# Kernel optimization log

Hardware: AMD Instinct MI355X
Metric: run time of the kernel (lower is better)

## Reference

```python
import jax, jax.numpy as jnp
import numpy as np

NEG_SLOPE = 0.2
EPS = 1e-5

N_NODES = 50000
N_GRAPHS = 500
NODES_PER_GRAPH = 100
N_EDGES = 500000
F_IN = 16
F_GRAPH = 4
HID = 64
N_CLASSES = 2


def setup_inputs() -> dict:
    key = jax.random.key(0)
    ks = jax.random.split(key, 32)
    x = jax.random.normal(ks[0], (N_NODES, F_IN), dtype=jnp.float32)
    # intra-graph random edges: dst lives in the same 100-node block as src
    src = jax.random.randint(ks[1], (N_EDGES,), 0, N_NODES)
    dst = (src // NODES_PER_GRAPH) * NODES_PER_GRAPH + jax.random.randint(ks[2], (N_EDGES,), 0, NODES_PER_GRAPH)
    edge_index = jnp.stack([src, dst]).astype(jnp.int64)
    graph_input = jax.random.normal(ks[3], (N_GRAPHS, F_GRAPH), dtype=jnp.float32)
    batch = (jnp.arange(N_NODES) // NODES_PER_GRAPH).astype(jnp.int64)

    def w(k, shape, scale=0.1):
        return (jax.random.normal(k, shape, dtype=jnp.float32) * scale)

    inp = dict(x=x, edge_index=edge_index, graph_input=graph_input, batch=batch)
    # GraphNorm params
    inp['gn_w'] = jnp.ones((F_IN,), jnp.float32)
    inp['gn_b'] = w(ks[4], (F_IN,))
    inp['gn_ms'] = jnp.ones((F_IN,), jnp.float32)
    inp['W1'] = w(ks[5], (F_IN, 4 * HID))
    inp['as1'] = w(ks[6], (4, HID)); inp['ad1'] = w(ks[7], (4, HID))
    inp['b1'] = w(ks[8], (4 * HID,))
    inp['W2'] = w(ks[9], (4 * HID, 4 * HID))
    inp['as2'] = w(ks[10], (4, HID)); inp['ad2'] = w(ks[11], (4, HID))
    inp['b2'] = w(ks[12], (4 * HID,))
    inp['W3'] = w(ks[13], (4 * HID, HID))
    inp['as3'] = w(ks[14], (1, HID)); inp['ad3'] = w(ks[15], (1, HID))
    inp['b3'] = w(ks[16], (HID,))
    # BatchNorm1d (eval mode) over [HID + F_GRAPH]
    D = HID + F_GRAPH
    inp['bn_g'] = 1.0 + w(ks[17], (D,))
    inp['bn_b'] = w(ks[18], (D,))
    inp['bn_m'] = jnp.zeros((D,), jnp.float32)
    inp['bn_v'] = jnp.ones((D,), jnp.float32)
    # Dense head
    inp['Wd1'] = w(ks[19], (D, HID)); inp['bd1'] = w(ks[20], (HID,))
    inp['Wd2'] = w(ks[21], (HID, HID)); inp['bd2'] = w(ks[22], (HID,))
    inp['Wo'] = w(ks[23], (HID, N_CLASSES)); inp['bo'] = w(ks[24], (N_CLASSES,))
    return inp


def _segment_softmax(e, seg, n):
    m = jax.ops.segment_max(e, seg, num_segments=n)
    ex = jnp.exp(e - m[seg])
    s = jax.ops.segment_sum(ex, seg, num_segments=n)
    return ex / s[seg]


def _gat_conv(x, src, dst, W, att_src, att_dst, b):
    N = x.shape[0]
    H, C = att_src.shape
    loop = jnp.arange(N)
    src = jnp.concatenate([src, loop])  # PyG GATConv adds self-loops
    dst = jnp.concatenate([dst, loop])
    h = (x @ W).reshape(N, H, C)
    a_src = (h * att_src).sum(-1)  # [N,H]
    a_dst = (h * att_dst).sum(-1)
    e = jax.nn.leaky_relu(a_src[src] + a_dst[dst], NEG_SLOPE)  # [E,H]
    alpha = _segment_softmax(e, dst, N)
    out = jax.ops.segment_sum(h[src] * alpha[:, :, None], dst, num_segments=N)
    return out.reshape(N, H * C) + b


def _graph_norm(x, batch, n_graphs, w, b, ms):
    cnt = jax.ops.segment_sum(jnp.ones((x.shape[0],), x.dtype), batch, num_segments=n_graphs)[:, None]
    mean = jax.ops.segment_sum(x, batch, num_segments=n_graphs) / cnt
    out = x - mean[batch] * ms
    var = jax.ops.segment_sum(out * out, batch, num_segments=n_graphs) / cnt
    return w * out / jnp.sqrt(var[batch] + EPS) + b


def _global_mean_pool(x, batch, n_graphs):
    cnt = jax.ops.segment_sum(jnp.ones((x.shape[0],), x.dtype), batch, num_segments=n_graphs)[:, None]
    return jax.ops.segment_sum(x, batch, num_segments=n_graphs) / cnt


def reference(x, edge_index, graph_input, batch,
              gn_w, gn_b, gn_ms,
              W1, as1, ad1, b1,
              W2, as2, ad2, b2,
              W3, as3, ad3, b3,
              bn_g, bn_b, bn_m, bn_v,
              Wd1, bd1, Wd2, bd2, Wo, bo):
    src, dst = edge_index[0], edge_index[1]
    G = graph_input.shape[0]
    h = _graph_norm(x, batch, G, gn_w, gn_b, gn_ms)
    # dropout is a no-op in eval
    h = jax.nn.elu(_gat_conv(h, src, dst, W1, as1, ad1, b1))
    h = jax.nn.elu(_gat_conv(h, src, dst, W2, as2, ad2, b2))
    h = _gat_conv(h, src, dst, W3, as3, ad3, b3)
    g = _global_mean_pool(h, batch, G)
    g = jnp.concatenate([g, graph_input], axis=1)
    g = (g - bn_m) / jnp.sqrt(bn_v + EPS) * bn_g + bn_b  # BatchNorm1d eval
    g = jax.nn.selu(g @ Wd1 + bd1)
    g = jax.nn.selu(g @ Wd2 + bd2)
    g = g @ Wo + bo
    return jax.nn.softmax(g, axis=1)
```

## Files before the change

### kernel.cpp

```cpp
#include <hip/hip_runtime.h>
#include <math.h>

#define N_NODES 50000
#define N_ROWS_PAD 50048
#define N_GRAPHS 500
#define NPG 100
#define N_EDGES 500000
#define F_IN 16
#define HID 64
#define EW_CAP 1408

#define SELU_SCALE 1.0507009873554804934193349852946f
#define SELU_ALPHA 1.6732632423543772848170429916717f

typedef __attribute__((ext_vector_type(8))) short short8;
typedef __attribute__((ext_vector_type(8))) unsigned short ushort8;
typedef __attribute__((ext_vector_type(4))) float floatx4;

__device__ __forceinline__ float lrelu(float x){ return x > 0.f ? x : 0.2f * x; }
__device__ __forceinline__ float eluf(float x){ return x > 0.f ? x : expf(x) - 1.f; }
__device__ __forceinline__ float seluf(float x){
    return x > 0.f ? SELU_SCALE * x : SELU_SCALE * (SELU_ALPHA * (expf(x) - 1.f));
}
__device__ __forceinline__ unsigned short f2bf(float x){
    unsigned u = __float_as_uint(x);
    return (unsigned short)((u + 0x7FFFu + ((u >> 16) & 1u)) >> 16);
}
__device__ __forceinline__ float bf2f(unsigned short u){
    return __uint_as_float((unsigned)u << 16);
}
__device__ __forceinline__ float bf2f_lo(unsigned u){
    return __uint_as_float(u << 16);
}
__device__ __forceinline__ float bf2f_hi(unsigned u){
    return __uint_as_float(u & 0xFFFF0000u);
}

__global__ void k_count(const int* __restrict__ dst, int* __restrict__ counts){
    int e = blockIdx.x * 256 + threadIdx.x;
    if (e < N_EDGES) atomicAdd(&counts[dst[e]], 1);
}

__global__ void __launch_bounds__(128)
k_local_scan(const int* __restrict__ counts, int* __restrict__ noff,
             int* __restrict__ cnt, int* __restrict__ write_ptr){
    __shared__ int s[128];
    int g = blockIdx.x, t = threadIdx.x;
    int v = (t < NPG) ? counts[g * NPG + t] : 0;
    s[t] = v; __syncthreads();
    for (int o = 1; o < 128; o <<= 1){
        int x = (t >= o) ? s[t - o] : 0;
        __syncthreads();
        s[t] += x;
        __syncthreads();
    }
    if (t < NPG){
        int excl = s[t] - v;
        noff[g * NPG + t] = excl;
        cnt[g * NPG + t] = v;
        write_ptr[g * NPG + t] = excl;
    }
}

__global__ void k_scatter(const int* __restrict__ src, const int* __restrict__ dst,
                          int* __restrict__ write_ptr, unsigned* __restrict__ csr){
    int e = blockIdx.x * 256 + threadIdx.x;
    if (e < N_EDGES){
        int d = dst[e];
        int g = d / NPG;
        int b = g * NPG;
        int pos = atomicAdd(&write_ptr[d], 1);
        csr[(size_t)g * EW_CAP + pos] = (unsigned)((src[e] - b) | ((d - b) << 8));
    }
}

__global__ void k_prep(const float* __restrict__ W1, const float* __restrict__ as1,
                       const float* __restrict__ ad1,
                       const float* __restrict__ W2, const float* __restrict__ as2,
                       const float* __restrict__ ad2,
                       const float* __restrict__ W3, const float* __restrict__ as3,
                       const float* __restrict__ ad3,
                       unsigned short* __restrict__ Wp2, unsigned short* __restrict__ Wp3,
                       float* __restrict__ M1f,
                       unsigned short* __restrict__ Mp2, unsigned short* __restrict__ Mp3){
    int id = blockIdx.x * 256 + threadIdx.x;
    if (id < 65536){
        int k = id >> 8, o = id & 255;
        int srccol = (o & 3) * 64 + (o >> 2);
        Wp2[(((k >> 3) * 256) + o) * 8 + (k & 7)] = f2bf(W2[k * 256 + srccol]);
    } else if (id < 81920){
        int i = id - 65536;
        int k = i >> 6, n = i & 63;
        Wp3[(((k >> 3) * 64) + n) * 8 + (k & 7)] = f2bf(W3[i]);
    } else if (id < 82048){
        int i = id - 81920;
        int k = i >> 3, j = i & 7;
        int h = j & 3;
        const float* a = (j < 4) ? as1 : ad1;
        float s = 0.f;
        for (int c = 0; c < 64; c++) s += W1[k * 256 + h * 64 + c] * a[h * 64 + c];
        M1f[k * 8 + j] = s;
    } else if (id < 86144){
        int i = id - 82048;
        int k = i >> 4, col = i & 15;
        float s = 0.f;
        if (col < 8){
            int h = col & 3;
            const float* a = (col < 4) ? as2 : ad2;
            for (int c = 0; c < 64; c++) s += W2[k * 256 + h * 64 + c] * a[h * 64 + c];
        }
        Mp2[((k >> 3) * 16 + col) * 8 + (k & 7)] = f2bf(s);
    } else if (id < 90240){
        int i = id - 86144;
        int k = i >> 4, col = i & 15;
        float s = 0.f;
        if (col < 2){
            const float* a = (col == 0) ? as3 : ad3;
            for (int c = 0; c < 64; c++) s += W3[k * 64 + c] * a[c];
        }
        Mp3[((k >> 3) * 16 + col) * 8 + (k & 7)] = f2bf(s);
    }
}

__global__ void __launch_bounds__(256)
k_gnorm_conv1(const float* __restrict__ x, const float* __restrict__ w,
              const float* __restrict__ b, const float* __restrict__ ms,
              const float* __restrict__ W1, const float* __restrict__ M1f,
              unsigned short* __restrict__ Ybf, float* __restrict__ lg1){
    __shared__ float sx[NPG * F_IN];
    __shared__ float Ws[16][256];
    __shared__ float red[16][16];
    __shared__ float meanS[16], varS[16];
    int g = blockIdx.x, t = threadIdx.x;
    int base = g * NPG;
    for (int idx = t; idx < NPG * F_IN; idx += 256) sx[idx] = x[base * F_IN + idx];
    for (int i = t; i < 1024; i += 256)
        *(float4*)&Ws[0][i * 4] = *(const float4*)&W1[i * 4];
    __syncthreads();
    int f = t & 15, grp = t >> 4;
    float p = 0.f;
    for (int i = grp; i < NPG; i += 16) p += sx[i * 16 + f];
    red[grp][f] = p; __syncthreads();
    if (t < 16){
        float s = 0.f;
        for (int i = 0; i < 16; i++) s += red[i][t];
        meanS[t] = s * (1.f / 100.f);
    }
    __syncthreads();
    float mm = meanS[f] * ms[f];
    p = 0.f;
    for (int i = grp; i < NPG; i += 16){ float v = sx[i * 16 + f] - mm; p += v * v; }
    red[grp][f] = p; __syncthreads();
    if (t < 16){
        float s = 0.f;
        for (int i = 0; i < 16; i++) s += red[i][t];
        varS[t] = s * (1.f / 100.f);
    }
    __syncthreads();
    for (int idx = t; idx < NPG * F_IN; idx += 256){
        int ff = idx & 15;
        sx[idx] = w[ff] * (sx[idx] - meanS[ff] * ms[ff]) * rsqrtf(varS[ff] + 1e-5f) + b[ff];
    }
    __syncthreads();
    int c4 = t & 15, rsub = t >> 4;
    for (int n = rsub; n < NPG; n += 16){
        float acc[16];
        #pragma unroll
        for (int j = 0; j < 16; j++) acc[j] = 0.f;
        #pragma unroll
        for (int k = 0; k < 16; k++){
            float a_ = sx[n * 16 + k];
            float4 b0 = *(const float4*)&Ws[k][c4 * 4];
            float4 b1 = *(const float4*)&Ws[k][64 + c4 * 4];
            float4 b2 = *(const float4*)&Ws[k][128 + c4 * 4];
            float4 b3 = *(const float4*)&Ws[k][192 + c4 * 4];
            float bv[16] = {b0.x, b0.y, b0.z, b0.w, b1.x, b1.y, b1.z, b1.w,
                            b2.x, b2.y, b2.z, b2.w, b3.x, b3.y, b3.z, b3.w};
            #pragma unroll
            for (int j = 0; j < 16; j++) acc[j] = fmaf(a_, bv[j], acc[j]);
        }
        ushort8 ua, ub;
        #pragma unroll
        for (int m = 0; m < 8; m++){
            ua[m] = f2bf(acc[(m & 3) * 4 + (m >> 2)]);
            ub[m] = f2bf(acc[(m & 3) * 4 + 2 + (m >> 2)]);
        }
        size_t ob = (size_t)(base + n) * 256 + c4 * 16;
        *(ushort8*)&Ybf[ob]     = ua;
        *(ushort8*)&Ybf[ob + 8] = ub;
    }
    for (int i = t; i < NPG * 8; i += 256){
        int n = i >> 3, j = i & 7;
        float s = 0.f;
        #pragma unroll
        for (int ff = 0; ff < 16; ff++) s += sx[n * 16 + ff] * M1f[ff * 8 + j];
        lg1[(size_t)(base + n) * 8 + j] = s;
    }
}

__global__ void __launch_bounds__(512)
k_fused4(const unsigned short* __restrict__ hbf, const float* __restrict__ lg,
         const float* __restrict__ bias,
         const unsigned* __restrict__ csr, const int* __restrict__ noff,
         const int* __restrict__ cnt, unsigned short* __restrict__ out_bf){
    __shared__ __align__(16) unsigned int edl[EW_CAP][4];
    __shared__ __align__(16) float asrcl[NPG * 4], adstl[NPG * 4];
    __shared__ __align__(16) float wselfl[NPG * 4], rsuml[NPG * 4];
    __shared__ int offl[NPG], cntl[NPG];

    int g = blockIdx.x, t = threadIdx.x;
    int wave = t >> 6, lane = t & 63;
    int base = g * NPG;
    size_t ebeg = (size_t)g * EW_CAP;

    if (t < NPG){
        offl[t] = noff[base + t];
        cntl[t] = cnt[base + t];
        const float* lp = lg + (size_t)(base + t) * 8;
        *(float4*)&asrcl[t * 4] = *(const float4*)lp;
        *(float4*)&adstl[t * 4] = *(const float4*)(lp + 4);
    }
    __syncthreads();
    int eln = offl[NPG - 1] + cntl[NPG - 1];
    for (int i = t; i < eln; i += 512) edl[i][2] = csr[ebeg + i];
    __syncthreads();

    for (int i = t; i < eln; i += 512){
        unsigned sd = edl[i][2];
        int s = sd & 0xFF, d = sd >> 8;
        float4 av = *(const float4*)&asrcl[s * 4];
        float4 dv = *(const float4*)&adstl[d * 4];
        unsigned w0 = f2bf(expf(lrelu(av.x + dv.x)));
        unsigned w1 = f2bf(expf(lrelu(av.y + dv.y)));
        unsigned w2 = f2bf(expf(lrelu(av.z + dv.z)));
        unsigned w3 = f2bf(expf(lrelu(av.w + dv.w)));
        edl[i][0] = w0 | (w1 << 16);
        edl[i][1] = w2 | (w3 << 16);
    }
    __syncthreads();

    if (t < NPG){
        int d = t;
        float4 av = *(const float4*)&asrcl[d * 4];
        float4 dv = *(const float4*)&adstl[d * 4];
        float ws0 = expf(lrelu(av.x + dv.x));
        float ws1 = expf(lrelu(av.y + dv.y));
        float ws2 = expf(lrelu(av.z + dv.z));
        float ws3 = expf(lrelu(av.w + dv.w));
        float s0 = ws0, s1 = ws1, s2 = ws2, s3 = ws3;
        int ebg = offl[d], n = cntl[d];
        for (int j = 0; j < n; j++){
            uint2 v = *(const uint2*)&edl[ebg + j][0];
            s0 += bf2f_lo(v.x); s1 += bf2f_hi(v.x);
            s2 += bf2f_lo(v.y); s3 += bf2f_hi(v.y);
        }
        *(float4*)&wselfl[d * 4] = make_float4(ws0, ws1, ws2, ws3);
        *(float4*)&rsuml[d * 4]  = make_float4(1.f / s0, 1.f / s1, 1.f / s2, 1.f / s3);
    }
    __syncthreads();

    float b0 = bias[lane], b1 = bias[64 + lane], b2 = bias[128 + lane], b3 = bias[192 + lane];
    for (int d = wave; d < NPG; d += 8){
        float4 ws = *(const float4*)&wselfl[d * 4];
        float4 rs = *(const float4*)&rsuml[d * 4];
        ushort4 hv = *(const ushort4*)&hbf[(size_t)(base + d) * 256 + lane * 4];
        float a0 = ws.x * bf2f(hv.x);
        float a1 = ws.y * bf2f(hv.y);
        float a2 = ws.z * bf2f(hv.z);
        float a3 = ws.w * bf2f(hv.w);
        int ebg = offl[d], n = cntl[d];
        int j = 0;
        #pragma unroll 1
        for (; j + 4 <= n; j += 4){
            #pragma unroll
            for (int k = 0; k < 4; k++){
                uint4 v = *(const uint4*)&edl[ebg + j + k][0];
                int s = (int)(v.z & 0xFFu);
                ushort4 x = *(const ushort4*)&hbf[(size_t)(base + s) * 256 + lane * 4];
                a0 = fmaf(bf2f_lo(v.x), bf2f(x.x), a0);
                a1 = fmaf(bf2f_hi(v.x), bf2f(x.y), a1);
                a2 = fmaf(bf2f_lo(v.y), bf2f(x.z), a2);
                a3 = fmaf(bf2f_hi(v.y), bf2f(x.w), a3);
            }
        }
        for (; j < n; j++){
            uint4 v = *(const uint4*)&edl[ebg + j][0];
            int s = (int)(v.z & 0xFFu);
            ushort4 x = *(const ushort4*)&hbf[(size_t)(base + s) * 256 + lane * 4];
            a0 = fmaf(bf2f_lo(v.x), bf2f(x.x), a0);
            a1 = fmaf(bf2f_hi(v.x), bf2f(x.y), a1);
            a2 = fmaf(bf2f_lo(v.y), bf2f(x.z), a2);
            a3 = fmaf(bf2f_hi(v.y), bf2f(x.w), a3);
        }
        size_t ob = (size_t)(base + d) * 256 + lane;
        out_bf[ob]       = f2bf(eluf(a0 * rs.x + b0));
        out_bf[ob + 64]  = f2bf(eluf(a1 * rs.y + b1));
        out_bf[ob + 128] = f2bf(eluf(a2 * rs.z + b2));
        out_bf[ob + 192] = f2bf(eluf(a3 * rs.w + b3));
    }
}

__global__ void __launch_bounds__(512)
k_mid(const unsigned short* __restrict__ xbin, const unsigned short* __restrict__ Wp2,
      const unsigned short* __restrict__ Mp2, const float* __restrict__ bias,
      const unsigned* __restrict__ csr, const int* __restrict__ noff,
      const int* __restrict__ cnt, unsigned short* __restrict__ out_bf){
    __shared__ __align__(16) unsigned short hl[NPG * 256];
    __shared__ __align__(16) unsigned int edw[EW_CAP][2];
    __shared__ unsigned short eds[EW_CAP];
    __shared__ __align__(16) float asrcl[NPG * 4], adstl[NPG * 4];
    __shared__ __align__(16) float wselfl[NPG * 4], rsuml[NPG * 4];
    __shared__ int offl[NPG], cntl[NPG];

    int g = blockIdx.x, t = threadIdx.x;
    int wave = t >> 6, lane = t & 63;
    int base = g * NPG;
    size_t ebeg = (size_t)g * EW_CAP;

    if (wave < 7){
        int quad = lane >> 4, ln = lane & 15;
        floatx4 acc[16];
        #pragma unroll
        for (int f = 0; f < 16; f++) acc[f] = (floatx4){0.f, 0.f, 0.f, 0.f};
        floatx4 accL = (floatx4){0.f, 0.f, 0.f, 0.f};
        const unsigned short* aptr = xbin + (size_t)(base + wave * 16 + ln) * 256 + quad * 8;
        for (int kt = 0; kt < 256; kt += 32){
            short8 a = *(const short8*)(aptr + kt);
            int kc = (kt >> 3) + quad;
            #pragma unroll
            for (int f = 0; f < 16; f++){
                short8 bfr = *(const short8*)(Wp2 + ((size_t)kc * 256 + f * 16 + ln) * 8);
                acc[f] = __builtin_amdgcn_mfma_f32_16x16x32_bf16(a, bfr, acc[f], 0, 0, 0);
            }
            short8 m = *(const short8*)(Mp2 + ((size_t)kc * 16 + ln) * 8);
            accL = __builtin_amdgcn_mfma_f32_16x16x32_bf16(a, m, accL, 0, 0, 0);
        }
        int rowb = wave * 16 + quad * 4;
        #pragma unroll
        for (int f = 0; f < 16; f++){
            int col = f * 16 + ln;
            #pragma unroll
            for (int rg = 0; rg < 4; rg++){
                int row = rowb + rg;
                if (row < NPG) hl[row * 256 + col] = f2bf(acc[f][rg]);
            }
        }
        if (ln < 8){
            #pragma unroll
            for (int rg = 0; rg < 4; rg++){
                int row = rowb + rg;
                if (row < NPG){
                    if (ln < 4) asrcl[row * 4 + ln] = accL[rg];
                    else        adstl[row * 4 + (ln - 4)] = accL[rg];
                }
            }
        }
    } else {
        for (int i = lane; i < NPG; i += 64){
            offl[i] = noff[base + i];
            cntl[i] = cnt[base + i];
        }
        int el = noff[base + NPG - 1] + cnt[base + NPG - 1];
        for (int i = lane; i < el; i += 64) eds[i] = (unsigned short)csr[ebeg + i];
    }
    __syncthreads();
    int eln = offl[NPG - 1] + cntl[NPG - 1];

    for (int i = t; i < eln; i += 512){
        unsigned sd = eds[i];
        int s = sd & 0xFF, d = sd >> 8;
        float4 av = *(const float4*)&asrcl[s * 4];
        float4 dv = *(const float4*)&adstl[d * 4];
        unsigned w0 = f2bf(expf(lrelu(av.x + dv.x)));
        unsigned w1 = f2bf(expf(lrelu(av.y + dv.y)));
        unsigned w2 = f2bf(expf(lrelu(av.z + dv.z)));
        unsigned w3 = f2bf(expf(lrelu(av.w + dv.w)));
        edw[i][0] = w0 | (w1 << 16);
        edw[i][1] = w2 | (w3 << 16);
    }
    __syncthreads();

    if (t < NPG){
        int d = t;
        float4 av = *(const float4*)&asrcl[d * 4];
        float4 dv = *(const float4*)&adstl[d * 4];
        float ws0 = expf(lrelu(av.x + dv.x));
        float ws1 = expf(lrelu(av.y + dv.y));
        float ws2 = expf(lrelu(av.z + dv.z));
        float ws3 = expf(lrelu(av.w + dv.w));
        float s0 = ws0, s1 = ws1, s2 = ws2, s3 = ws3;
        int ebg = offl[d], n = cntl[d];
        for (int j = 0; j < n; j++){
            uint2 v = *(const uint2*)&edw[ebg + j][0];
            s0 += bf2f_lo(v.x); s1 += bf2f_hi(v.x);
            s2 += bf2f_lo(v.y); s3 += bf2f_hi(v.y);
        }
        *(float4*)&wselfl[d * 4] = make_float4(ws0, ws1, ws2, ws3);
        *(float4*)&rsuml[d * 4]  = make_float4(1.f / s0, 1.f / s1, 1.f / s2, 1.f / s3);
    }
    __syncthreads();

    float b0 = bias[lane], b1 = bias[64 + lane], b2 = bias[128 + lane], b3 = bias[192 + lane];
    for (int d = wave; d < NPG; d += 8){
        float4 ws = *(const float4*)&wselfl[d * 4];
        float4 rs = *(const float4*)&rsuml[d * 4];
        ushort4 hv = *(const ushort4*)&hl[d * 256 + lane * 4];
        float a0 = ws.x * bf2f(hv.x);
        float a1 = ws.y * bf2f(hv.y);
        float a2 = ws.z * bf2f(hv.z);
        float a3 = ws.w * bf2f(hv.w);
        int ebg = offl[d], n = cntl[d];
        int j = 0;
        #pragma unroll 1
        for (; j + 4 <= n; j += 4){
            #pragma unroll
            for (int k = 0; k < 4; k++){
                int s = (int)(eds[ebg + j + k] & 0xFFu);
                uint2 v = *(const uint2*)&edw[ebg + j + k][0];
                ushort4 x = *(const ushort4*)&hl[s * 256 + lane * 4];
                a0 = fmaf(bf2f_lo(v.x), bf2f(x.x), a0);
                a1 = fmaf(bf2f_hi(v.x), bf2f(x.y), a1);
                a2 = fmaf(bf2f_lo(v.y), bf2f(x.z), a2);
                a3 = fmaf(bf2f_hi(v.y), bf2f(x.w), a3);
            }
        }
        for (; j < n; j++){
            int s = (int)(eds[ebg + j] & 0xFFu);
            uint2 v = *(const uint2*)&edw[ebg + j][0];
            ushort4 x = *(const ushort4*)&hl[s * 256 + lane * 4];
            a0 = fmaf(bf2f_lo(v.x), bf2f(x.x), a0);
            a1 = fmaf(bf2f_hi(v.x), bf2f(x.y), a1);
            a2 = fmaf(bf2f_lo(v.y), bf2f(x.z), a2);
            a3 = fmaf(bf2f_hi(v.y), bf2f(x.w), a3);
        }
        size_t ob = (size_t)(base + d) * 256 + lane;
        out_bf[ob]       = f2bf(eluf(a0 * rs.x + b0));
        out_bf[ob + 64]  = f2bf(eluf(a1 * rs.y + b1));
        out_bf[ob + 128] = f2bf(eluf(a2 * rs.z + b2));
        out_bf[ob + 192] = f2bf(eluf(a3 * rs.w + b3));
    }
}

__global__ void __launch_bounds__(512)
k_tail(const unsigned short* __restrict__ xb, const unsigned short* __restrict__ Wp3,
       const unsigned short* __restrict__ Mp3, const float* __restrict__ bias,
       const unsigned* __restrict__ csr, const int* __restrict__ noff,
       const int* __restrict__ cnt, const float* __restrict__ gin,
       const float* __restrict__ bn_g, const float* __restrict__ bn_b,
       const float* __restrict__ bn_m, const float* __restrict__ bn_v,
       const float* __restrict__ Wd1, const float* __restrict__ bd1,
       const float* __restrict__ Wd2, const float* __restrict__ bd2,
       const float* __restrict__ Wo, const float* __restrict__ bo,
       float* __restrict__ out){
    __shared__ __align__(16) unsigned short h3[NPG * 64];
    __shared__ __align__(16) unsigned int edl[EW_CAP][2];
    __shared__ float asrcl[NPG], adstl[NPG];
    __shared__ float wselfl[NPG], rsuml[NPG];
    __shared__ int offl[NPG], cntl[NPG];
    __shared__ float red[8][64];
    __shared__ float gv[68], g2[64], g3[64];

    int g = blockIdx.x, t = threadIdx.x;
    int wave = t >> 6, lane = t & 63;
    int base = g * NPG;
    size_t ebeg = (size_t)g * EW_CAP;

    if (wave < 7){
        int quad = lane >> 4, ln = lane & 15;
        floatx4 acc[4];
        #pragma unroll
        for (int f = 0; f < 4; f++) acc[f] = (floatx4){0.f, 0.f, 0.f, 0.f};
        floatx4 accL = (floatx4){0.f, 0.f, 0.f, 0.f};
        const unsigned short* aptr = xb + (size_t)(base + wave * 16 + ln) * 256 + quad * 8;
        for (int kt = 0; kt < 256; kt += 32){
            short8 a = *(const short8*)(aptr + kt);
            int kc = (kt >> 3) + quad;
            #pragma unroll
            for (int f = 0; f < 4; f++){
                short8 bfr = *(const short8*)(Wp3 + ((size_t)kc * 64 + f * 16 + ln) * 8);
                acc[f] = __builtin_amdgcn_mfma_f32_16x16x32_bf16(a, bfr, acc[f], 0, 0, 0);
            }
            short8 m = *(const short8*)(Mp3 + ((size_t)kc * 16 + ln) * 8);
            accL = __builtin_amdgcn_mfma_f32_16x16x32_bf16(a, m, accL, 0, 0, 0);
        }
        int rowb = wave * 16 + quad * 4;
        #pragma unroll
        for (int f = 0; f < 4; f++){
            int col = f * 16 + ln;
            #pragma unroll
            for (int rg = 0; rg < 4; rg++){
                int row = rowb + rg;
                if (row < NPG) h3[row * 64 + col] = f2bf(acc[f][rg]);
            }
        }
        if (ln < 2){
            #pragma unroll
            for (int rg = 0; rg < 4; rg++){
                int row = rowb + rg;
                if (row < NPG){
                    if (ln == 0) asrcl[row] = accL[rg];
                    else         adstl[row] = accL[rg];
                }
            }
        }
    } else {
        for (int i = lane; i < NPG; i += 64){
            offl[i] = noff[base + i];
            cntl[i] = cnt[base + i];
        }
        int el = noff[base + NPG - 1] + cnt[base + NPG - 1];
        for (int i = lane; i < el; i += 64) edl[i][1] = csr[ebeg + i];
    }
    __syncthreads();
    int eln = offl[NPG - 1] + cntl[NPG - 1];

    for (int i = t; i < eln; i += 512){
        unsigned sd = edl[i][1];
        int s = sd & 0xFF, d = sd >> 8;
        edl[i][0] = (unsigned)f2bf(expf(lrelu(asrcl[s] + adstl[d])));
    }
    __syncthreads();

    if (t < NPG){
        float wsf = expf(lrelu(asrcl[t] + adstl[t]));
        float sum = wsf;
        int ebg = offl[t], n = cntl[t];
        for (int j = 0; j < n; j++) sum += bf2f((unsigned short)edl[ebg + j][0]);
        wselfl[t] = wsf;
        rsuml[t] = 1.f / sum;
    }
    __syncthreads();

    float bl = bias[lane];
    float pool = 0.f;
    for (int d = wave; d < NPG; d += 8){
        float acc = wselfl[d] * bf2f(h3[d * 64 + lane]);
        int ebg = offl[d], n = cntl[d];
        for (int j = 0; j < n; j++){
            uint2 v = *(const uint2*)&edl[ebg + j][0];
            acc = fmaf(bf2f_lo(v.x), bf2f(h3[(int)(v.y & 0xFFu) * 64 + lane]), acc);
        }
        pool += acc * rsuml[d] + bl;
    }
    red[wave][lane] = pool;
    __syncthreads();

    if (t < 64){
        float s = 0.f;
        #pragma unroll
        for (int i = 0; i < 8; i++) s += red[i][t];
        float mean = s * (1.f / 100.f);
        gv[t] = (mean - bn_m[t]) * rsqrtf(bn_v[t] + 1e-5f) * bn_g[t] + bn_b[t];
    } else if (t < 68){
        int j = t - 64;
        float v = gin[g * 4 + j];
        gv[t] = (v - bn_m[t]) * rsqrtf(bn_v[t] + 1e-5f) * bn_g[t] + bn_b[t];
    }
    __syncthreads();
    if (t < 64){
        float s = bd1[t];
        for (int i = 0; i < 68; i++) s += gv[i] * Wd1[i * 64 + t];
        g2[t] = seluf(s);
    }
    __syncthreads();
    if (t < 64){
        float s = bd2[t];
        for (int i = 0; i < 64; i++) s += g2[i] * Wd2[i * 64 + t];
        g3[t] = seluf(s);
    }
    __syncthreads();
    if (t == 0){
        float l0 = bo[0], l1 = bo[1];
        for (int i = 0; i < 64; i++){ l0 += g3[i] * Wo[i * 2]; l1 += g3[i] * Wo[i * 2 + 1]; }
        float mx = fmaxf(l0, l1);
        float e0 = expf(l0 - mx), e1 = expf(l1 - mx);
        float inv = 1.f / (e0 + e1);
        out[g * 2] = e0 * inv;
        out[g * 2 + 1] = e1 * inv;
    }
}

extern "C" void kernel_launch(void* const* d_in, const int* in_sizes, int n_in,
                              void* d_out, int out_size, void* d_ws, size_t ws_size,
                              hipStream_t stream){
    const float* x   = (const float*)d_in[0];
    const int*   ei  = (const int*)d_in[1];
    const float* gin = (const float*)d_in[2];
    const float* gn_w = (const float*)d_in[4];
    const float* gn_b = (const float*)d_in[5];
    const float* gn_ms = (const float*)d_in[6];
    const float* W1 = (const float*)d_in[7];
    const float* as1 = (const float*)d_in[8];
    const float* ad1 = (const float*)d_in[9];
    const float* b1 = (const float*)d_in[10];
    const float* W2 = (const float*)d_in[11];
    const float* as2 = (const float*)d_in[12];
    const float* ad2 = (const float*)d_in[13];
    const float* b2 = (const float*)d_in[14];
    const float* W3 = (const float*)d_in[15];
    const float* as3 = (const float*)d_in[16];
    const float* ad3 = (const float*)d_in[17];
    const float* b3 = (const float*)d_in[18];
    const float* bn_g = (const float*)d_in[19];
    const float* bn_b = (const float*)d_in[20];
    const float* bn_m = (const float*)d_in[21];
    const float* bn_v = (const float*)d_in[22];
    const float* Wd1 = (const float*)d_in[23];
    const float* bd1 = (const float*)d_in[24];
    const float* Wd2 = (const float*)d_in[25];
    const float* bd2 = (const float*)d_in[26];
    const float* Wo = (const float*)d_in[27];
    const float* bo = (const float*)d_in[28];
    float* out = (float*)d_out;

    const int* src = ei;
    const int* dst = ei + N_EDGES;

    char* ws = (char*)d_ws;
    size_t off = 0;
    auto alloc = [&](size_t bytes) -> void* {
        void* p = ws + off;
        off = (off + bytes + 255) & ~(size_t)255;
        return p;
    };
    int* counts     = (int*)alloc((size_t)N_NODES * 4);
    int* write_ptr  = (int*)alloc((size_t)N_NODES * 4);
    unsigned* csr   = (unsigned*)alloc((size_t)N_GRAPHS * EW_CAP * 4);
    int* noff       = (int*)alloc((size_t)N_NODES * 4);
    int* cnt        = (int*)alloc((size_t)N_NODES * 4);
    unsigned short* wp2 = (unsigned short*)alloc((size_t)256 * 256 * 2);
    unsigned short* wp3 = (unsigned short*)alloc((size_t)256 * 64 * 2);
    float* M1f      = (float*)alloc((size_t)16 * 8 * 4);
    unsigned short* Mp2 = (unsigned short*)alloc((size_t)32 * 16 * 8 * 2);
    unsigned short* Mp3 = (unsigned short*)alloc((size_t)32 * 16 * 8 * 2);
    float* lg1      = (float*)alloc((size_t)N_NODES * 8 * 4);
    unsigned short* xbh = (unsigned short*)alloc((size_t)N_ROWS_PAD * 256 * 2);
    unsigned short* xb  = (unsigned short*)alloc((size_t)N_ROWS_PAD * 256 * 2);

    hipMemsetAsync(counts, 0, (size_t)N_NODES * 4, stream);
    k_count<<<(N_EDGES + 255) / 256, 256, 0, stream>>>(dst, counts);
    k_prep<<<(90240 + 255) / 256, 256, 0, stream>>>(W1, as1, ad1, W2, as2, ad2,
                                                    W3, as3, ad3, wp2, wp3, M1f, Mp2, Mp3);
    k_local_scan<<<N_GRAPHS, 128, 0, stream>>>(counts, noff, cnt, write_ptr);
    k_scatter<<<(N_EDGES + 255) / 256, 256, 0, stream>>>(src, dst, write_ptr, csr);

    k_gnorm_conv1<<<N_GRAPHS, 256, 0, stream>>>(x, gn_w, gn_b, gn_ms, W1, M1f, xbh, lg1);
    k_fused4<<<N_GRAPHS, 512, 0, stream>>>(xbh, lg1, b1, csr, noff, cnt, xb);

    k_mid<<<N_GRAPHS, 512, 0, stream>>>(xb, wp2, Mp2, b2, csr, noff, cnt, xbh);

    k_tail<<<N_GRAPHS, 512, 0, stream>>>(xbh, wp3, Mp3, b3, csr, noff, cnt, gin,
                                         bn_g, bn_b, bn_m, bn_v,
                                         Wd1, bd1, Wd2, bd2, Wo, bo, out);
}
```

Baseline: 307.7 us.

## Repartition layer-2 MFMA GEMM by output columns with register-resident weights

```diff
diff --git a/kernel.cpp b/kernel.cpp
--- a/kernel.cpp
+++ b/kernel.cpp
@@ -314,38 +314,45 @@
 
     int g = blockIdx.x, t = threadIdx.x;
     int wave = t >> 6, lane = t & 63;
+    int quad = lane >> 4, ln = lane & 15;
     int base = g * NPG;
     size_t ebeg = (size_t)g * EW_CAP;
 
-    if (wave < 7){
-        int quad = lane >> 4, ln = lane & 15;
-        floatx4 acc[16];
-        #pragma unroll
-        for (int f = 0; f < 16; f++) acc[f] = (floatx4){0.f, 0.f, 0.f, 0.f};
+    int f0 = wave * 2, f1 = wave * 2 + 1;
+    short8 bw0[8], bw1[8];
+    #pragma unroll
+    for (int s = 0; s < 8; s++){
+        int kc = 4 * s + quad;
+        bw0[s] = *(const short8*)(Wp2 + ((size_t)kc * 256 + f0 * 16 + ln) * 8);
+        bw1[s] = *(const short8*)(Wp2 + ((size_t)kc * 256 + f1 * 16 + ln) * 8);
+    }
+
+    for (int tile = 0; tile < 7; tile++){
+        const unsigned short* aptr = xbin + (size_t)(base + tile * 16 + ln) * 256 + quad * 8;
+        floatx4 acc0 = (floatx4){0.f, 0.f, 0.f, 0.f};
+        floatx4 acc1 = (floatx4){0.f, 0.f, 0.f, 0.f};
         floatx4 accL = (floatx4){0.f, 0.f, 0.f, 0.f};
-        const unsigned short* aptr = xbin + (size_t)(base + wave * 16 + ln) * 256 + quad * 8;
-        for (int kt = 0; kt < 256; kt += 32){
-            short8 a = *(const short8*)(aptr + kt);
-            int kc = (kt >> 3) + quad;
-            #pragma unroll
-            for (int f = 0; f < 16; f++){
-                short8 bfr = *(const short8*)(Wp2 + ((size_t)kc * 256 + f * 16 + ln) * 8);
-                acc[f] = __builtin_amdgcn_mfma_f32_16x16x32_bf16(a, bfr, acc[f], 0, 0, 0);
-            }
-            short8 m = *(const short8*)(Mp2 + ((size_t)kc * 16 + ln) * 8);
-            accL = __builtin_amdgcn_mfma_f32_16x16x32_bf16(a, m, accL, 0, 0, 0);
-        }
-        int rowb = wave * 16 + quad * 4;
-        #pragma unroll
-        for (int f = 0; f < 16; f++){
-            int col = f * 16 + ln;
-            #pragma unroll
-            for (int rg = 0; rg < 4; rg++){
-                int row = rowb + rg;
-                if (row < NPG) hl[row * 256 + col] = f2bf(acc[f][rg]);
-            }
-        }
-        if (ln < 8){
+        #pragma unroll
+        for (int s = 0; s < 8; s++){
+            short8 a = *(const short8*)(aptr + s * 32);
+            acc0 = __builtin_amdgcn_mfma_f32_16x16x32_bf16(a, bw0[s], acc0, 0, 0, 0);
+            acc1 = __builtin_amdgcn_mfma_f32_16x16x32_bf16(a, bw1[s], acc1, 0, 0, 0);
+            if (wave == 7){
+                int kc = 4 * s + quad;
+                short8 m = *(const short8*)(Mp2 + ((size_t)kc * 16 + ln) * 8);
+                accL = __builtin_amdgcn_mfma_f32_16x16x32_bf16(a, m, accL, 0, 0, 0);
+            }
+        }
+        int rowb = tile * 16 + quad * 4;
+        #pragma unroll
+        for (int rg = 0; rg < 4; rg++){
+            int row = rowb + rg;
+            if (row < NPG){
+                hl[row * 256 + f0 * 16 + ln] = f2bf(acc0[rg]);
+                hl[row * 256 + f1 * 16 + ln] = f2bf(acc1[rg]);
+            }
+        }
+        if (wave == 7 && ln < 8){
             #pragma unroll
             for (int rg = 0; rg < 4; rg++){
                 int row = rowb + rg;
@@ -355,16 +362,15 @@
                 }
             }
         }
-    } else {
-        for (int i = lane; i < NPG; i += 64){
-            offl[i] = noff[base + i];
-            cntl[i] = cnt[base + i];
-        }
-        int el = noff[base + NPG - 1] + cnt[base + NPG - 1];
-        for (int i = lane; i < el; i += 64) eds[i] = (unsigned short)csr[ebeg + i];
-    }
-    __syncthreads();
-    int eln = offl[NPG - 1] + cntl[NPG - 1];
+    }
+    if (t < NPG){
+        offl[t] = noff[base + t];
+        cntl[t] = cnt[base + t];
+    }
+    int el = noff[base + NPG - 1] + cnt[base + NPG - 1];
+    for (int i = t; i < el; i += 512) eds[i] = (unsigned short)csr[ebeg + i];
+    __syncthreads();
+    int eln = el;
 
     for (int i = t; i < eln; i += 512){
         unsigned sd = eds[i];
```

Measured after the change: 316.1 us. 2.7% more time.
